# Kernel tuning notes

Measured on AMD Instinct MI355X. Metric: run time of the kernel, lower is better.

## Reference

```python
import jax, jax.numpy as jnp
import numpy as np

EMB_SIZE = 768
BLOCK_SIZE = 64
NUM_CLASS = 97
N = 4096
NUM_BLOCKS = EMB_SIZE // BLOCK_SIZE  # 12


def setup_inputs() -> dict:
    key = jax.random.key(0)
    k1, k2, k3 = jax.random.split(key, 3)
    head_embeddings = jax.random.normal(k1, (N, EMB_SIZE), dtype=jnp.float32)
    tail_embeddings = jax.random.normal(k2, (N, EMB_SIZE), dtype=jnp.float32)
    # xavier_uniform for [NUM_CLASS, EMB_SIZE*BLOCK_SIZE]
    fan_in = EMB_SIZE * BLOCK_SIZE
    fan_out = NUM_CLASS
    bound = float(np.sqrt(6.0 / (fan_in + fan_out)))
    W = jax.random.uniform(k3, (NUM_CLASS, EMB_SIZE * BLOCK_SIZE), dtype=jnp.float32,
                           minval=-bound, maxval=bound)
    b = jnp.full((NUM_CLASS,), 0.1, dtype=jnp.float32)
    return {"head_embeddings": head_embeddings, "tail_embeddings": tail_embeddings,
            "W": W, "b": b}


def reference(head_embeddings, tail_embeddings, W, b):
    n = head_embeddings.shape[0]
    b1 = head_embeddings.reshape(n, NUM_BLOCKS, BLOCK_SIZE)  # [N, K, S]
    b2 = tail_embeddings.reshape(n, NUM_BLOCKS, BLOCK_SIZE)  # [N, K, S]
    # block-wise outer product: [N, K, S, S] -> [N, K*S*S]
    bl = jnp.einsum('nki,nkj->nkij', b1, b2).reshape(n, EMB_SIZE * BLOCK_SIZE)
    logits = bl @ W.T + b  # [N, NUM_CLASS]
    return logits
```

## Files before the change

### kernel.cpp

```cpp
#include <hip/hip_runtime.h>
#include <hip/hip_bf16.h>
#include <stdint.h>

#define NROWS 4096
#define NCLS  97
#define EMB   768
#define KTOT  49152
#define OUT_ELEMS (NROWS * NCLS)
#define NK32  (KTOT / 32)
#define WT_BYTES ((size_t)NK32 * 128 * 64)

typedef __attribute__((ext_vector_type(8)))  short short8;
typedef __attribute__((ext_vector_type(4)))  float floatx4;
typedef __bf16 bf16x2 __attribute__((ext_vector_type(2)));
typedef __bf16 bf16x8 __attribute__((ext_vector_type(8)));

__device__ __forceinline__ uint32_t pkmul(uint32_t a, uint32_t b) {
  bf16x2 x = __builtin_bit_cast(bf16x2, a);
  bf16x2 y = __builtin_bit_cast(bf16x2, b);
  bf16x2 r = x * y;
  return __builtin_bit_cast(uint32_t, r);
}

__device__ __forceinline__ uint4 cvt8(float4 a, float4 b) {
  bf16x8 v;
  v[0] = (__bf16)a.x; v[1] = (__bf16)a.y; v[2] = (__bf16)a.z; v[3] = (__bf16)a.w;
  v[4] = (__bf16)b.x; v[5] = (__bf16)b.y; v[6] = (__bf16)b.z; v[7] = (__bf16)b.w;
  return __builtin_bit_cast(uint4, v);
}

__global__ void prep_wt(const float* __restrict__ W, uint4* __restrict__ wt)
{
  const int nwt = NK32 * 128 * 4;
  int t = blockIdx.x * blockDim.x + threadIdx.x;
  if (t >= nwt) return;
  int eo = t & 3;
  int c  = (t >> 2) & 127;
  int kc = t >> 9;
  uint4 v = uint4{0u, 0u, 0u, 0u};
  if (c < NCLS) {
    const float4* p = (const float4*)(W + (size_t)c * KTOT + kc * 32 + eo * 8);
    v = cvt8(p[0], p[1]);
  }
  wt[t] = v;
}

__global__ __launch_bounds__(256, 2)
void bilinear_main(const float* __restrict__ b1g,
                   const float* __restrict__ b2g,
                   const char* __restrict__ Wt,
                   const float* __restrict__ biasg,
                   float* __restrict__ P,
                   float* __restrict__ outd,
                   int klen, int nslice, int G)
{
  const int tid  = threadIdx.x;
  const int w    = tid >> 6;
  const int l    = tid & 63;
  const int l15  = l & 15;
  const int quad = l >> 4;
  const int mhalf = w & 1;
  const int chalf = w >> 1;

  const int n = blockIdx.x;
  int s, bm;
  if (G > 0) { s = (n & 7) + 8 * ((n >> 3) % G); bm = (n >> 3) / G; }
  else       { s = n % nslice;                   bm = n / nslice; }
  const int k0 = s * klen;

  int nrow[4];
#pragma unroll
  for (int rt = 0; rt < 4; ++rt) nrow[rt] = bm * 128 + mhalf * 64 + rt * 16 + l15;

  const char* wtl = Wt + (size_t)(k0 >> 5) * 8192
                       + (chalf * 64 + l15) * 64 + quad * 16;

  floatx4 acc[4][4];
#pragma unroll
  for (int rt = 0; rt < 4; ++rt)
#pragma unroll
    for (int ct = 0; ct < 4; ++ct)
      acc[rt][ct] = floatx4{0.f, 0.f, 0.f, 0.f};

  uint4 b2c[4][2];
  uint4 b1c[4];
  int cur_k = -1;
  const int nwin = klen >> 6;

  for (int gwin = 0; gwin < nwin; gwin += 8) {
    const int kap0 = k0 + (gwin << 6);
    const int kblk = kap0 >> 12;
    const int i0   = (kap0 >> 6) & 63;
    if (kblk != cur_k) {
      cur_k = kblk;
#pragma unroll
      for (int rt = 0; rt < 4; ++rt)
#pragma unroll
        for (int kh = 0; kh < 2; ++kh) {
          const float* p = b2g + (size_t)nrow[rt] * EMB +
                           kblk * 64 + kh * 32 + quad * 8;
          b2c[rt][kh] = cvt8(((const float4*)p)[0], ((const float4*)p)[1]);
        }
    }
#pragma unroll
    for (int rt = 0; rt < 4; ++rt) {
      const float* p = b1g + (size_t)nrow[rt] * EMB + kblk * 64 + i0;
      b1c[rt] = cvt8(((const float4*)p)[0], ((const float4*)p)[1]);
    }

#pragma unroll
    for (int ii = 0; ii < 8; ++ii) {
      const char* pw = wtl + (size_t)(gwin + ii) * 16384;

      uint32_t s2[4];
#pragma unroll
      for (int rt = 0; rt < 4; ++rt) {
        uint32_t d = (&b1c[rt].x)[ii >> 1];
        uint32_t h = (ii & 1) ? (d >> 16) : (d & 0xffffu);
        s2[rt] = h | (h << 16);
      }

#pragma unroll
      for (int kh = 0; kh < 2; ++kh) {
        short8 wf[4];
#pragma unroll
        for (int ct = 0; ct < 4; ++ct)
          wf[ct] = __builtin_bit_cast(short8,
                     *(const uint4*)(pw + kh * 8192 + ct * 1024));
        uint4 afr[4];
#pragma unroll
        for (int rt = 0; rt < 4; ++rt) {
          afr[rt].x = pkmul(s2[rt], b2c[rt][kh].x);
          afr[rt].y = pkmul(s2[rt], b2c[rt][kh].y);
          afr[rt].z = pkmul(s2[rt], b2c[rt][kh].z);
          afr[rt].w = pkmul(s2[rt], b2c[rt][kh].w);
        }
#pragma unroll
        for (int rt = 0; rt < 4; ++rt) {
          short8 af = __builtin_bit_cast(short8, afr[rt]);
#pragma unroll
          for (int ct = 0; ct < 4; ++ct)
            acc[rt][ct] = __builtin_amdgcn_mfma_f32_16x16x32_bf16(
                              af, wf[ct], acc[rt][ct], 0, 0, 0);
        }
      }
    }
  }

  if (P) {
    float* Pb = P + (size_t)s * OUT_ELEMS;
#pragma unroll
    for (int rt = 0; rt < 4; ++rt)
#pragma unroll
      for (int ct = 0; ct < 4; ++ct) {
        const int c = chalf * 64 + ct * 16 + l15;
        if (c < NCLS) {
#pragma unroll
          for (int r = 0; r < 4; ++r) {
            const int row = bm * 128 + mhalf * 64 + rt * 16 + quad * 4 + r;
            Pb[(size_t)row * NCLS + c] = acc[rt][ct][r];
          }
        }
      }
  } else {
#pragma unroll
    for (int rt = 0; rt < 4; ++rt)
#pragma unroll
      for (int ct = 0; ct < 4; ++ct) {
        const int c = chalf * 64 + ct * 16 + l15;
        if (c < NCLS) {
          const float bv = biasg[c];
#pragma unroll
          for (int r = 0; r < 4; ++r) {
            const int row = bm * 128 + mhalf * 64 + rt * 16 + quad * 4 + r;
            outd[(size_t)row * NCLS + c] = acc[rt][ct][r] + bv;
          }
        }
      }
  }
}

__global__ void reduce_bias(const float* __restrict__ P,
                            const float* __restrict__ biasg,
                            float* __restrict__ out, int KS)
{
  int i = blockIdx.x * blockDim.x + threadIdx.x;
  const int n4 = OUT_ELEMS / 4;
  if (i >= n4) return;
  int c0 = (i * 4) % NCLS;
  int c1 = c0 + 1 == NCLS ? 0 : c0 + 1;
  int c2 = c1 + 1 == NCLS ? 0 : c1 + 1;
  int c3 = c2 + 1 == NCLS ? 0 : c2 + 1;
  float4 s;
  s.x = biasg[c0]; s.y = biasg[c1]; s.z = biasg[c2]; s.w = biasg[c3];
  const float4* P4 = (const float4*)P;
  for (int t = 0; t < KS; ++t) {
    float4 v = P4[(size_t)t * n4 + i];
    s.x += v.x; s.y += v.y; s.z += v.z; s.w += v.w;
  }
  ((float4*)out)[i] = s;
}

extern "C" void kernel_launch(void* const* d_in, const int* in_sizes, int n_in,
                              void* d_out, int out_size, void* d_ws, size_t ws_size,
                              hipStream_t stream) {
  const float* b1f = (const float*)d_in[0];
  const float* b2f = (const float*)d_in[1];
  const float* Wf  = (const float*)d_in[2];
  const float* bbf = (const float*)d_in[3];
  float* out = (float*)d_out;

  const size_t slice = (size_t)OUT_ELEMS * 4;
  static const int cands[] = {32, 24, 16, 12, 8, 6, 4, 3, 2, 1};
  int KS = 0;
  for (int i = 0; i < 10; ++i)
    if (WT_BYTES + (size_t)cands[i] * slice <= ws_size) { KS = cands[i]; break; }

  uint4* Wt = (uint4*)d_ws;
  const int nwt = NK32 * 128 * 4;
  prep_wt<<<(nwt + 255) / 256, 256, 0, stream>>>(Wf, Wt);

  if (KS > 0) {
    float* P = (float*)((char*)d_ws + WT_BYTES);
    const int G = (KS % 8 == 0) ? KS / 8 : 0;
    bilinear_main<<<dim3(KS * 32), 256, 0, stream>>>(
        b1f, b2f, (const char*)Wt, bbf, P, nullptr, KTOT / KS, KS, G);
    reduce_bias<<<(OUT_ELEMS / 4 + 255) / 256, 256, 0, stream>>>(P, bbf, out, KS);
  } else {
    bilinear_main<<<dim3(32), 256, 0, stream>>>(
        b1f, b2f, (const char*)Wt, bbf, nullptr, out, KTOT, 1, 0);
  }
}
```

Baseline: 172.8 us.

## Give each wave all 128 rows and 32 classes, cap split-K at 16

The warp tiling changes from 2x2 waves (64 rows x 64 classes each) to 1x4 waves (128 rows x 32 classes each). Each wave now builds outer-product A fragments for 8 row tiles and loads only 2 W fragments per step, which cuts redundant W loads but doubles the per-wave pkmul work and the register footprint of the b1/b2 caches. The largest split-K candidate drops from 32 to 16, so fewer blocks launch and fewer partial slices go to the reduce. The grid becomes 2D (bm, slice), which removes the earlier G-based slice interleaving used for cache locality.

```diff
diff --git a/kernel.cpp b/kernel.cpp
--- a/kernel.cpp
+++ b/kernel.cpp
@@ -52,38 +52,33 @@
                    const float* __restrict__ biasg,
                    float* __restrict__ P,
                    float* __restrict__ outd,
-                   int klen, int nslice, int G)
+                   int klen)
 {
   const int tid  = threadIdx.x;
   const int w    = tid >> 6;
   const int l    = tid & 63;
   const int l15  = l & 15;
   const int quad = l >> 4;
-  const int mhalf = w & 1;
-  const int chalf = w >> 1;
-
-  const int n = blockIdx.x;
-  int s, bm;
-  if (G > 0) { s = (n & 7) + 8 * ((n >> 3) % G); bm = (n >> 3) / G; }
-  else       { s = n % nslice;                   bm = n / nslice; }
+  const int bm = blockIdx.x;
+  const int s  = blockIdx.y;
   const int k0 = s * klen;
 
-  int nrow[4];
-#pragma unroll
-  for (int rt = 0; rt < 4; ++rt) nrow[rt] = bm * 128 + mhalf * 64 + rt * 16 + l15;
+  int nrow[8];
+#pragma unroll
+  for (int rt = 0; rt < 8; ++rt) nrow[rt] = bm * 128 + rt * 16 + l15;
 
   const char* wtl = Wt + (size_t)(k0 >> 5) * 8192
-                       + (chalf * 64 + l15) * 64 + quad * 16;
-
-  floatx4 acc[4][4];
-#pragma unroll
-  for (int rt = 0; rt < 4; ++rt)
-#pragma unroll
-    for (int ct = 0; ct < 4; ++ct)
+                       + (w * 32 + l15) * 64 + quad * 16;
+
+  floatx4 acc[8][2];
+#pragma unroll
+  for (int rt = 0; rt < 8; ++rt)
+#pragma unroll
+    for (int ct = 0; ct < 2; ++ct)
       acc[rt][ct] = floatx4{0.f, 0.f, 0.f, 0.f};
 
-  uint4 b2c[4][2];
-  uint4 b1c[4];
+  uint4 b2c[8][2];
+  uint4 b1c[8];
   int cur_k = -1;
   const int nwin = klen >> 6;
 
@@ -94,7 +89,7 @@
     if (kblk != cur_k) {
       cur_k = kblk;
 #pragma unroll
-      for (int rt = 0; rt < 4; ++rt)
+      for (int rt = 0; rt < 8; ++rt)
 #pragma unroll
         for (int kh = 0; kh < 2; ++kh) {
           const float* p = b2g + (size_t)nrow[rt] * EMB +
@@ -103,7 +98,7 @@
         }
     }
 #pragma unroll
-    for (int rt = 0; rt < 4; ++rt) {
+    for (int rt = 0; rt < 8; ++rt) {
       const float* p = b1g + (size_t)nrow[rt] * EMB + kblk * 64 + i0;
       b1c[rt] = cvt8(((const float4*)p)[0], ((const float4*)p)[1]);
     }
@@ -112,9 +107,9 @@
     for (int ii = 0; ii < 8; ++ii) {
       const char* pw = wtl + (size_t)(gwin + ii) * 16384;
 
-      uint32_t s2[4];
-#pragma unroll
-      for (int rt = 0; rt < 4; ++rt) {
+      uint32_t s2[8];
+#pragma unroll
+      for (int rt = 0; rt < 8; ++rt) {
         uint32_t d = (&b1c[rt].x)[ii >> 1];
         uint32_t h = (ii & 1) ? (d >> 16) : (d & 0xffffu);
         s2[rt] = h | (h << 16);
@@ -122,24 +117,21 @@
 
 #pragma unroll
       for (int kh = 0; kh < 2; ++kh) {
-        short8 wf[4];
-#pragma unroll
-        for (int ct = 0; ct < 4; ++ct)
+        short8 wf[2];
+#pragma unroll
+        for (int ct = 0; ct < 2; ++ct)
           wf[ct] = __builtin_bit_cast(short8,
                      *(const uint4*)(pw + kh * 8192 + ct * 1024));
-        uint4 afr[4];
-#pragma unroll
-        for (int rt = 0; rt < 4; ++rt) {
-          afr[rt].x = pkmul(s2[rt], b2c[rt][kh].x);
-          afr[rt].y = pkmul(s2[rt], b2c[rt][kh].y);
-          afr[rt].z = pkmul(s2[rt], b2c[rt][kh].z);
-          afr[rt].w = pkmul(s2[rt], b2c[rt][kh].w);
-        }
-#pragma unroll
-        for (int rt = 0; rt < 4; ++rt) {
-          short8 af = __builtin_bit_cast(short8, afr[rt]);
-#pragma unroll
-          for (int ct = 0; ct < 4; ++ct)
+#pragma unroll
+        for (int rt = 0; rt < 8; ++rt) {
+          uint4 afr;
+          afr.x = pkmul(s2[rt], b2c[rt][kh].x);
+          afr.y = pkmul(s2[rt], b2c[rt][kh].y);
+          afr.z = pkmul(s2[rt], b2c[rt][kh].z);
+          afr.w = pkmul(s2[rt], b2c[rt][kh].w);
+          short8 af = __builtin_bit_cast(short8, afr);
+#pragma unroll
+          for (int ct = 0; ct < 2; ++ct)
             acc[rt][ct] = __builtin_amdgcn_mfma_f32_16x16x32_bf16(
                               af, wf[ct], acc[rt][ct], 0, 0, 0);
         }
@@ -150,29 +142,29 @@
   if (P) {
     float* Pb = P + (size_t)s * OUT_ELEMS;
 #pragma unroll
-    for (int rt = 0; rt < 4; ++rt)
-#pragma unroll
-      for (int ct = 0; ct < 4; ++ct) {
-        const int c = chalf * 64 + ct * 16 + l15;
+    for (int rt = 0; rt < 8; ++rt)
+#pragma unroll
+      for (int ct = 0; ct < 2; ++ct) {
+        const int c = w * 32 + ct * 16 + l15;
         if (c < NCLS) {
 #pragma unroll
           for (int r = 0; r < 4; ++r) {
-            const int row = bm * 128 + mhalf * 64 + rt * 16 + quad * 4 + r;
+            const int row = bm * 128 + rt * 16 + quad * 4 + r;
             Pb[(size_t)row * NCLS + c] = acc[rt][ct][r];
           }
         }
       }
   } else {
 #pragma unroll
-    for (int rt = 0; rt < 4; ++rt)
-#pragma unroll
-      for (int ct = 0; ct < 4; ++ct) {
-        const int c = chalf * 64 + ct * 16 + l15;
+    for (int rt = 0; rt < 8; ++rt)
+#pragma unroll
+      for (int ct = 0; ct < 2; ++ct) {
+        const int c = w * 32 + ct * 16 + l15;
         if (c < NCLS) {
           const float bv = biasg[c];
 #pragma unroll
           for (int r = 0; r < 4; ++r) {
-            const int row = bm * 128 + mhalf * 64 + rt * 16 + quad * 4 + r;
+            const int row = bm * 128 + rt * 16 + quad * 4 + r;
             outd[(size_t)row * NCLS + c] = acc[rt][ct][r] + bv;
           }
         }
@@ -211,9 +203,9 @@
   float* out = (float*)d_out;
 
   const size_t slice = (size_t)OUT_ELEMS * 4;
-  static const int cands[] = {32, 24, 16, 12, 8, 6, 4, 3, 2, 1};
+  static const int cands[] = {16, 12, 8, 6, 4, 3, 2, 1};
   int KS = 0;
-  for (int i = 0; i < 10; ++i)
+  for (int i = 0; i < 8; ++i)
     if (WT_BYTES + (size_t)cands[i] * slice <= ws_size) { KS = cands[i]; break; }
 
   uint4* Wt = (uint4*)d_ws;
@@ -222,12 +214,11 @@
 
   if (KS > 0) {
     float* P = (float*)((char*)d_ws + WT_BYTES);
-    const int G = (KS % 8 == 0) ? KS / 8 : 0;
-    bilinear_main<<<dim3(KS * 32), 256, 0, stream>>>(
-        b1f, b2f, (const char*)Wt, bbf, P, nullptr, KTOT / KS, KS, G);
+    bilinear_main<<<dim3(32, KS), 256, 0, stream>>>(
+        b1f, b2f, (const char*)Wt, bbf, P, nullptr, KTOT / KS);
     reduce_bias<<<(OUT_ELEMS / 4 + 255) / 256, 256, 0, stream>>>(P, bbf, out, KS);
   } else {
-    bilinear_main<<<dim3(32), 256, 0, stream>>>(
-        b1f, b2f, (const char*)Wt, bbf, nullptr, out, KTOT, 1, 0);
-  }
-}
+    bilinear_main<<<dim3(32, 1), 256, 0, stream>>>(
+        b1f, b2f, (const char*)Wt, bbf, nullptr, out, KTOT);
+  }
+}
```

Result: slower. 315.3 us (+82.4%).
